# Kernel tuning notes

Measured on AMD Instinct MI355X. Metric: run time of the kernel, lower is better.

## Reference

```python
import jax, jax.numpy as jnp
import numpy as np
from jax import lax

N_NODES = 100000
N_EDGES = 3200000
NODE_DIM = 128
K = 8            # number of kmeans heads
MAX_OVERLAP = 2  # top-k cluster memberships per node
THRESH = 1e-8


def setup_inputs() -> dict:
    key = jax.random.key(0)
    k1, k2, k3, k4, k5 = jax.random.split(key, 5)
    x = jax.random.normal(k1, (N_NODES, NODE_DIM), dtype=jnp.float32)
    edge_index = jax.random.randint(k2, (2, N_EDGES), 0, N_NODES, dtype=jnp.int64)
    # binary initial cluster-membership masks [N, K] (float, like KMeansCarry.mask)
    mask = (jax.random.uniform(k3, (N_NODES, K)) > 0.5).astype(jnp.float32)
    Ww = jax.random.normal(k4, (K, NODE_DIM, NODE_DIM), dtype=jnp.float32) * (1.0 / np.sqrt(NODE_DIM))
    Wm = jax.random.normal(k5, (K, NODE_DIM, 1), dtype=jnp.float32) * (1.0 / np.sqrt(NODE_DIM))
    return {"x": x, "edge_index": edge_index, "mask": mask, "Ww": Ww, "Wm": Wm}


def reference(x, edge_index, mask, Ww, Wm):
    """KMeans over graph: k heads -> boolean node scores -> norm-weighted top-k assignment."""
    N = x.shape[0]
    src, dst = edge_index[0], edge_index[1]

    def head(m_col, Ww_i, Wm_i):
        # masked node features (KMeansCarry.masked_x)
        xm = x * m_col[:, None]                                   # [N, D]
        node_mask = m_col > 0                                     # [N]
        # masked subgraph (KMeansCarry.masked_edge_index): keep edges with both endpoints in mask
        ev = (node_mask[src] & node_mask[dst]).astype(x.dtype)    # [E]
        # weighting module: per-node transform
        w = jax.nn.relu(xm @ Ww_i)                                # [N, D]
        # message passing over masked subgraph (irregular gather/scatter)
        agg = jax.ops.segment_sum(w[src] * ev[:, None], dst, num_segments=N)  # [N, D]
        # mask module score -> act -> threshold at 0 (KMeansHead.forward)
        score = ((xm + agg) @ Wm_i)[:, 0]                         # [N]
        return jnp.tanh(score) > 0                                # bool [N]

    # vmap over the K heads
    head_masks = jax.vmap(head, in_axes=(1, 0, 0), out_axes=1)(mask, Ww, Wm)  # [N, K] bool

    # KMeans.forward combine step
    above_thresh = head_masks  # bool > THRESH (1e-8 < 1) == the bool itself
    norms = jnp.linalg.norm(x, axis=1, keepdims=True)             # [N, 1]
    masked_weights = jnp.where(above_thresh, norms, -jnp.inf)     # [N, K]
    top_vals, top_idx = lax.top_k(masked_weights, MAX_OVERLAP)    # [N, MAX_OVERLAP]
    valid = jnp.isfinite(top_vals)
    # scatter ones at (row, top_idx) where valid  (duplicate-safe via one-hot + min)
    oh = jax.nn.one_hot(top_idx, K, dtype=x.dtype) * valid[..., None].astype(x.dtype)
    final_mask = jnp.minimum(oh.sum(axis=1), 1.0)                 # [N, K]
    return final_mask
```

## Files before the change

kernel.cpp:

```cpp
#include <hip/hip_runtime.h>

#define N_NODES 100000
#define N_EDGES 3200000
#define D 128
#define K 8

#define TAU 4e-3f
#define WL_CAP 262144

#define CHUNK 128
#define GWAVES 8

#define BKT 256
#define NB  ((N_NODES + BKT - 1) / BKT)
#define EPB 16384
#define NEB ((N_EDGES + EPB - 1) / EPB)

typedef float  f32x4  __attribute__((ext_vector_type(4)));
typedef __bf16 bf16x8 __attribute__((ext_vector_type(8)));

static __device__ __forceinline__ unsigned short bfbits(float f)
{
    const __bf16 b = (__bf16)f;
    return __builtin_bit_cast(unsigned short, b);
}
static __device__ __forceinline__ float bfback(unsigned short u)
{
    return (float)__builtin_bit_cast(__bf16, u);
}

__global__ __launch_bounds__(256)
void compact_kernel(const float* __restrict__ mask,
                    int* __restrict__ lists,
                    int* __restrict__ cnts,
                    unsigned char* __restrict__ mb)
{
    __shared__ int wcnt[4][K];
    __shared__ int wbase[4][K];

    const int n = blockIdx.x * 256 + threadIdx.x;
    const int lane = threadIdx.x & 63;
    const int wave = threadIdx.x >> 6;
    const bool valid = (n < N_NODES);

    unsigned long long ball[K];
    int bits8 = 0;
    #pragma unroll
    for (int k = 0; k < K; ++k) {
        const bool m = valid && (mask[(size_t)n * K + k] > 0.0f);
        bits8 |= m ? (1 << k) : 0;
        ball[k] = __ballot(m);
        if (lane == 0) wcnt[wave][k] = __popcll(ball[k]);
    }
    __syncthreads();

    if (threadIdx.x < K) {
        const int k = threadIdx.x;
        const int t0 = wcnt[0][k], t1 = wcnt[1][k], t2 = wcnt[2][k], t3 = wcnt[3][k];
        const int base = (t0 + t1 + t2 + t3)
                       ? atomicAdd(&cnts[k], t0 + t1 + t2 + t3) : 0;
        wbase[0][k] = base;
        wbase[1][k] = base + t0;
        wbase[2][k] = base + t0 + t1;
        wbase[3][k] = base + t0 + t1 + t2;
    }
    __syncthreads();

    #pragma unroll
    for (int k = 0; k < K; ++k) {
        if ((ball[k] >> lane) & 1ull) {
            const int pos = __popcll(ball[k] & ((1ull << lane) - 1ull));
            lists[(size_t)k * N_NODES + wbase[wave][k] + pos] = n;
        }
    }
    if (valid) mb[n] = (unsigned char)bits8;
}

__global__ __launch_bounds__(256)
void wsplit_kernel(const float* __restrict__ Ww,
                   unsigned short* __restrict__ wtH,
                   unsigned short* __restrict__ wtL)
{
    const int t = blockIdx.x * 256 + threadIdx.x;
    if (t >= K * D * D) return;
    const int k   = t >> 14;
    const int kk  = (t >> 7) & 127;
    const int col = t & 127;
    const float v = Ww[t];
    const __bf16 h = (__bf16)v;
    const __bf16 l = (__bf16)(v - (float)h);
    const int o = (k << 14) | (col << 7) | kk;
    wtH[o] = __builtin_bit_cast(unsigned short, h);
    wtL[o] = __builtin_bit_cast(unsigned short, l);
}

__global__ __launch_bounds__(512, 4)
void head_gemm_kernel(const float* __restrict__ x,
                      const unsigned short* __restrict__ wtH,
                      const unsigned short* __restrict__ wtL,
                      const float* __restrict__ Wm,
                      const int* __restrict__ lists,
                      const int* __restrict__ cnts,
                      float* __restrict__ t32,
                      float* __restrict__ base32)
{
    __shared__ __align__(16) unsigned short Ah[CHUNK * D];
    __shared__ __align__(16) unsigned short Al[CHUNK * D];
    __shared__ float redT[GWAVES][64];
    __shared__ float redB[CHUNK][4];
    __shared__ int   ids[CHUNK];

    const int bid = blockIdx.x;
    const int k = (bid >> 3) & 7;
    const int c = ((bid >> 6) << 3) | (bid & 7);

    const int cnt = cnts[k];
    const int nbase = c * CHUNK;
    if (nbase >= cnt) return;

    const int tid = threadIdx.x;
    const int lane = tid & 63;
    const int wave = __builtin_amdgcn_readfirstlane((int)(tid >> 6));
    const int* list = lists + (size_t)k * N_NODES;

    if (tid < CHUNK) {
        int idx = nbase + tid;
        if (idx >= cnt) idx = cnt - 1;
        ids[tid] = list[idx];
    }
    __syncthreads();

    {
        const int r = tid >> 2;
        const int q = tid & 3;
        const int id = ids[r];
        const float4* xr  = (const float4*)(x + (size_t)id * D);
        const float4* wm4 = (const float4*)(Wm + k * D);
        float bp = 0.0f;
        #pragma unroll
        for (int i = 0; i < 8; ++i) {
            const int f4 = q + 4 * i;
            const float4 v  = xr[f4];
            const float4 wv = wm4[f4];
            bp += v.x * wv.x + v.y * wv.y + v.z * wv.z + v.w * wv.w;
            ushort4 h, l;
            h.x = bfbits(v.x); l.x = bfbits(v.x - bfback(h.x));
            h.y = bfbits(v.y); l.y = bfbits(v.y - bfback(h.y));
            h.z = bfbits(v.z); l.z = bfbits(v.z - bfback(h.z));
            h.w = bfbits(v.w); l.w = bfbits(v.w - bfback(h.w));
            const int boff = ((r * 256 + f4 * 8) ^ ((r & 7) << 4)) >> 1;
            *(ushort4*)&Ah[boff] = h;
            *(ushort4*)&Al[boff] = l;
        }
        redB[r][q] = bp;
    }
    __syncthreads();

    const int wm_ = wave >> 2;
    const int wn  = wave & 3;
    const int l15 = lane & 15;
    const int lg  = lane >> 4;
    const int n0  = wn * 32;

    f32x4 acc[4][2];
    #pragma unroll
    for (int mf = 0; mf < 4; ++mf) {
        acc[mf][0] = (f32x4){0.f, 0.f, 0.f, 0.f};
        acc[mf][1] = (f32x4){0.f, 0.f, 0.f, 0.f};
    }

    const unsigned short* bH0 = wtH + (((k * D + n0 + l15) << 7) + 8 * lg);
    const unsigned short* bH1 = bH0 + (16 << 7);
    const unsigned short* bL0 = wtL + (((k * D + n0 + l15) << 7) + 8 * lg);
    const unsigned short* bL1 = bL0 + (16 << 7);

    #pragma unroll
    for (int s = 0; s < 4; ++s) {
        const int ko = s * 32;
        const bf16x8 Bh0 = *reinterpret_cast<const bf16x8*>(bH0 + ko);
        const bf16x8 Bh1 = *reinterpret_cast<const bf16x8*>(bH1 + ko);
        const bf16x8 Bl0 = *reinterpret_cast<const bf16x8*>(bL0 + ko);
        const bf16x8 Bl1 = *reinterpret_cast<const bf16x8*>(bL1 + ko);
        #pragma unroll
        for (int mf = 0; mf < 4; ++mf) {
            const int m = wm_ * 64 + mf * 16 + l15;
            const int byt = (m * 256 + (ko + 8 * lg) * 2) ^ ((m & 7) << 4);
            const bf16x8 Amh = *reinterpret_cast<const bf16x8*>(&Ah[byt >> 1]);
            const bf16x8 Aml = *reinterpret_cast<const bf16x8*>(&Al[byt >> 1]);
            acc[mf][0] = __builtin_amdgcn_mfma_f32_16x16x32_bf16(Amh, Bh0, acc[mf][0], 0, 0, 0);
            acc[mf][1] = __builtin_amdgcn_mfma_f32_16x16x32_bf16(Amh, Bh1, acc[mf][1], 0, 0, 0);
            acc[mf][0] = __builtin_amdgcn_mfma_f32_16x16x32_bf16(Amh, Bl0, acc[mf][0], 0, 0, 0);
            acc[mf][1] = __builtin_amdgcn_mfma_f32_16x16x32_bf16(Amh, Bl1, acc[mf][1], 0, 0, 0);
            acc[mf][0] = __builtin_amdgcn_mfma_f32_16x16x32_bf16(Aml, Bh0, acc[mf][0], 0, 0, 0);
            acc[mf][1] = __builtin_amdgcn_mfma_f32_16x16x32_bf16(Aml, Bh1, acc[mf][1], 0, 0, 0);
        }
    }

    const float wmv0 = Wm[k * D + n0 + l15];
    const float wmv1 = Wm[k * D + n0 + 16 + l15];
    float keep = 0.0f;
    #pragma unroll
    for (int mf = 0; mf < 4; ++mf) {
        #pragma unroll
        for (int r = 0; r < 4; ++r) {
            float p = fmaxf(acc[mf][0][r], 0.0f) * wmv0
                    + fmaxf(acc[mf][1][r], 0.0f) * wmv1;
            p += __shfl_xor(p, 1);
            p += __shfl_xor(p, 2);
            p += __shfl_xor(p, 4);
            p += __shfl_xor(p, 8);
            if (l15 == mf * 4 + r) keep = p;
        }
    }
    redT[wave][((l15 >> 2) << 4) + (lg << 2) + (l15 & 3)] = keep;
    __syncthreads();

    if (tid < CHUNK) {
        const int r = tid;
        const int idx = nbase + r;
        if (idx < cnt) {
            const int wg = r >> 6;
            const int rl = r & 63;
            const float ts = redT[wg * 4 + 0][rl] + redT[wg * 4 + 1][rl]
                           + redT[wg * 4 + 2][rl] + redT[wg * 4 + 3][rl];
            const float bs = redB[r][0] + redB[r][1] + redB[r][2] + redB[r][3];
            const int id = ids[r];
            t32[(size_t)id * K + k]    = ts;
            base32[(size_t)id * K + k] = bs;
        }
    }
}

__global__ __launch_bounds__(256)
void ehist_kernel(const int* __restrict__ ei, int* __restrict__ bhist)
{
    __shared__ int lh[NB];
    const int tid = threadIdx.x;
    for (int i = tid; i < NB; i += 256) lh[i] = 0;
    __syncthreads();
    const int e0 = blockIdx.x * EPB;
    #pragma unroll 4
    for (int i = 0; i < EPB / 256; ++i) {
        const int e = e0 + i * 256 + tid;
        if (e < N_EDGES) {
            const int d = ei[(long long)N_EDGES + e];
            atomicAdd(&lh[d >> 8], 1);
        }
    }
    __syncthreads();
    for (int i = tid; i < NB; i += 256) {
        const int c = lh[i];
        if (c) atomicAdd(&bhist[i], c);
    }
}

__global__ __launch_bounds__(512)
void escan_kernel(const int* __restrict__ bhist,
                  int* __restrict__ bases,
                  int* __restrict__ cursors)
{
    __shared__ int sc[512];
    const int tid = threadIdx.x;
    const int v = (tid < NB) ? bhist[tid] : 0;
    sc[tid] = v;
    __syncthreads();
    for (int off = 1; off < 512; off <<= 1) {
        int t = 0;
        if (tid >= off) t = sc[tid - off];
        __syncthreads();
        sc[tid] += t;
        __syncthreads();
    }
    if (tid < NB) {
        const int ex = sc[tid] - v;
        bases[tid]   = ex;
        cursors[tid] = ex;
        if (tid == NB - 1) bases[NB] = sc[tid];
    }
}

__global__ __launch_bounds__(256)
void ebucket_kernel(const int* __restrict__ ei,
                    int* __restrict__ cursors,
                    int* __restrict__ bkt)
{
    __shared__ int lh[NB];
    __shared__ int wb[NB];
    const int tid = threadIdx.x;
    for (int i = tid; i < NB; i += 256) lh[i] = 0;
    __syncthreads();
    const int e0 = blockIdx.x * EPB;
    #pragma unroll 4
    for (int i = 0; i < EPB / 256; ++i) {
        const int e = e0 + i * 256 + tid;
        if (e < N_EDGES) atomicAdd(&lh[ei[(long long)N_EDGES + e] >> 8], 1);
    }
    __syncthreads();
    for (int i = tid; i < NB; i += 256) {
        const int c = lh[i];
        wb[i] = c ? atomicAdd(&cursors[i], c) : 0;
        lh[i] = 0;
    }
    __syncthreads();
    #pragma unroll 4
    for (int i = 0; i < EPB / 256; ++i) {
        const int e = e0 + i * 256 + tid;
        if (e < N_EDGES) {
            const int d = ei[(long long)N_EDGES + e];
            const int s = ei[e];
            const int b = d >> 8;
            const int r = atomicAdd(&lh[b], 1);
            const int idx = wb[b] + r;
            if (idx < N_EDGES)
                bkt[idx] = (s << 8) | (d & 255);
        }
    }
}

__global__ __launch_bounds__(512)
void eaccum_kernel(const int* __restrict__ bkt,
                   const int* __restrict__ bases,
                   const unsigned char* __restrict__ mb,
                   const float* __restrict__ t32,
                   const float* __restrict__ base32,
                   float* __restrict__ agg32,
                   float* __restrict__ out,
                   unsigned char* __restrict__ flag8,
                   double* __restrict__ s64,
                   int2* __restrict__ wl,
                   int* __restrict__ wlcnt)
{
    __shared__ float acc[BKT * K];
    __shared__ unsigned char mbl[BKT];
    __shared__ unsigned char fll[BKT];
    __shared__ int anyfl;
    const int b = blockIdx.x;
    const int n0 = b << 8;
    const int tid = threadIdx.x;
    for (int i = tid; i < BKT * K; i += 512) acc[i] = 0.0f;
    if (tid < BKT) {
        const int n = n0 + tid;
        mbl[tid] = (n < N_NODES) ? mb[n] : 0;
    }
    if (tid == 0) anyfl = 0;
    __syncthreads();

    const int eB = bases[b];
    int eE = bases[b + 1];
    if (eE > N_EDGES) eE = N_EDGES;
    for (int e = eB + tid; e < eE; e += 512) {
        const int rec = bkt[e];
        const int s  = rec >> 8;
        const int dl = rec & 255;
        const unsigned md = mbl[dl] & mb[s];
        if (md) {
            const float4* tr = (const float4*)(t32 + (size_t)s * K);
            const float4 t0 = tr[0], t1 = tr[1];
            #pragma unroll
            for (int k = 0; k < K; ++k) {
                const float tv = (k < 4)
                    ? ((k < 2) ? (k == 0 ? t0.x : t0.y) : (k == 2 ? t0.z : t0.w))
                    : ((k < 6) ? (k == 4 ? t1.x : t1.y) : (k == 6 ? t1.z : t1.w));
                if (((md >> k) & 1) && tv != 0.0f)
                    atomicAdd(&acc[(dl << 3) + k], tv);
            }
        }
    }
    __syncthreads();

    if (tid < BKT) {
        const int n = n0 + tid;
        if (n < N_NODES) {
            const unsigned m8 = mbl[tid];
            const float4* b4 = (const float4*)(base32 + (size_t)n * K);
            const float4 b40 = b4[0], b41 = b4[1];
            float bs[K];
            bs[0] = b40.x; bs[1] = b40.y; bs[2] = b40.z; bs[3] = b40.w;
            bs[4] = b41.x; bs[5] = b41.y; bs[6] = b41.z; bs[7] = b41.w;
            float o[K];
            int cnt = 0, fl = 0;
            #pragma unroll
            for (int k = 0; k < K; ++k) {
                const float sc = bs[k] + acc[(tid << 3) + k];
                const bool masked = (m8 >> k) & 1;
                const bool hm = masked && (sc > 0.0f);
                if (masked && fabsf(sc) < TAU) fl |= (1 << k);
                o[k] = (hm && cnt < 2) ? 1.0f : 0.0f;
                cnt += hm ? 1 : 0;
            }
            float4* op = (float4*)(out + (size_t)n * K);
            op[0] = make_float4(o[0], o[1], o[2], o[3]);
            op[1] = make_float4(o[4], o[5], o[6], o[7]);
            float4* ap = (float4*)(agg32 + (size_t)n * K);
            ap[0] = make_float4(acc[(tid << 3) + 0], acc[(tid << 3) + 1],
                                acc[(tid << 3) + 2], acc[(tid << 3) + 3]);
            ap[1] = make_float4(acc[(tid << 3) + 4], acc[(tid << 3) + 5],
                                acc[(tid << 3) + 6], acc[(tid << 3) + 7]);
            flag8[n] = (unsigned char)fl;
            fll[tid] = (unsigned char)fl;
            if (fl) {
                anyfl = 1;
                #pragma unroll
                for (int k = 0; k < K; ++k)
                    if ((fl >> k) & 1) s64[(size_t)n * K + k] = 0.0;
            }
        } else {
            fll[tid] = 0;
        }
    }
    __syncthreads();

    if (anyfl) {
        for (int e = eB + tid; e < eE; e += 512) {
            const int rec = bkt[e];
            const int dl = rec & 255;
            unsigned f = fll[dl];
            if (!f) continue;
            const int s = rec >> 8;
            f &= mb[s];
            while (f) {
                const int k = __ffs(f) - 1;
                f &= f - 1;
                const int idx = atomicAdd(wlcnt, 1);
                if (idx < WL_CAP) wl[idx] = make_int2(s | (k << 20), n0 + dl);
            }
        }
    }
}

__global__ __launch_bounds__(256)
void scatter_fallback_kernel(const int* __restrict__ ei,
                             const unsigned char* __restrict__ mb,
                             const float* __restrict__ t32,
                             float* __restrict__ agg32)
{
    const long long tid = (long long)blockIdx.x * 256 + threadIdx.x;
    if (tid >= (long long)N_EDGES * K) return;
    const int k = (int)(tid & (K - 1));
    const long long e = tid >> 3;
    const int d = ei[(long long)N_EDGES + e];
    const int s = ei[e];
    const unsigned md = mb[d] & mb[s];
    if (!((md >> k) & 1)) return;
    const float v = t32[(size_t)s * K + k];
    if (v != 0.0f) atomicAdd(&agg32[(size_t)d * K + k], v);
}

__global__ __launch_bounds__(256)
void combine_flag_kernel(const unsigned char* __restrict__ mb,
                         const float* __restrict__ base32,
                         const float* __restrict__ agg32,
                         float* __restrict__ out,
                         unsigned char* __restrict__ flag8,
                         double* __restrict__ s64)
{
    const int n = blockIdx.x * 256 + threadIdx.x;
    if (n >= N_NODES) return;
    const unsigned m8 = mb[n];
    float o[K];
    int cnt = 0, fl = 0;
    #pragma unroll
    for (int k = 0; k < K; ++k) {
        const float s = base32[(size_t)n * K + k] + agg32[(size_t)n * K + k];
        const bool masked = (m8 >> k) & 1;
        const bool hm = masked && (s > 0.0f);
        if (masked && fabsf(s) < TAU) fl |= (1 << k);
        o[k] = (hm && cnt < 2) ? 1.0f : 0.0f;
        cnt += hm ? 1 : 0;
    }
    float4* op = (float4*)(out + (size_t)n * K);
    op[0] = make_float4(o[0], o[1], o[2], o[3]);
    op[1] = make_float4(o[4], o[5], o[6], o[7]);
    flag8[n] = (unsigned char)fl;
    if (fl) {
        #pragma unroll
        for (int k = 0; k < K; ++k)
            if ((fl >> k) & 1) s64[(size_t)n * K + k] = 0.0;
    }
}

__global__ __launch_bounds__(256)
void edge_flag_kernel(const int* __restrict__ ei,
                      const unsigned char* __restrict__ mb,
                      const unsigned char* __restrict__ flag8,
                      int2* __restrict__ wl,
                      int* __restrict__ wlcnt)
{
    const int e = blockIdx.x * 256 + threadIdx.x;
    if (e >= N_EDGES) return;
    const int d = ei[(long long)N_EDGES + e];
    unsigned f = flag8[d];
    if (!f) return;
    const int s = ei[e];
    f &= mb[s];
    while (f) {
        const int k = __ffs(f) - 1;
        f &= f - 1;
        const int idx = atomicAdd(wlcnt, 1);
        if (idx < WL_CAP) wl[idx] = make_int2(s | (k << 20), d);
    }
}

__global__ __launch_bounds__(256)
void repair_t_kernel(const float* __restrict__ x,
                     const float* __restrict__ Ww,
                     const float* __restrict__ Wm,
                     const int2* __restrict__ wl,
                     const int* __restrict__ wlcnt,
                     double* __restrict__ score64)
{
    const int lane = threadIdx.x & 63;
    const int waveId = blockIdx.x * 4 + (threadIdx.x >> 6);
    const int nWaves = gridDim.x * 4;
    int cnt = *wlcnt;
    if (cnt > WL_CAP) cnt = WL_CAP;
    for (int w = waveId; w < cnt; w += nWaves) {
        const int2 ent = wl[w];
        const int s = __builtin_amdgcn_readfirstlane(ent.x & 0xFFFFF);
        const int k = __builtin_amdgcn_readfirstlane(ent.x >> 20);
        const int d = ent.y;
        const float* xr = x + (size_t)s * D;
        const float* Wk = Ww + (size_t)k * D * D;
        double c0 = 0.0, c1 = 0.0;
        for (int j = 0; j < D; ++j) {
            const double xd = (double)xr[j];
            c0 = fma(xd, (double)Wk[j * D + lane], c0);
            c1 = fma(xd, (double)Wk[j * D + lane + 64], c1);
        }
        double ts = fmax(c0, 0.0) * (double)Wm[k * D + lane]
                  + fmax(c1, 0.0) * (double)Wm[k * D + lane + 64];
        #pragma unroll
        for (int off = 32; off > 0; off >>= 1) ts += __shfl_xor(ts, off);
        if (lane == 0) atomicAdd(&score64[(size_t)d * K + k], ts);
    }
}

__global__ __launch_bounds__(256)
void repair_combine_kernel(const float* __restrict__ x,
                           const unsigned char* __restrict__ mb,
                           const float* __restrict__ Wm,
                           const float* __restrict__ base32,
                           const float* __restrict__ agg32,
                           const double* __restrict__ score64,
                           const unsigned char* __restrict__ flag8,
                           float* __restrict__ out)
{
    const int n = blockIdx.x * 256 + threadIdx.x;
    if (n >= N_NODES) return;
    const unsigned f = flag8[n];
    if (!f) return;
    const unsigned m8 = mb[n];
    float o[K];
    int cnt = 0;
    #pragma unroll
    for (int k = 0; k < K; ++k) {
        bool hm;
        if ((f >> k) & 1) {
            double b = 0.0;
            for (int j = 0; j < D; ++j)
                b = fma((double)x[(size_t)n * D + j], (double)Wm[k * D + j], b);
            hm = (b + score64[(size_t)n * K + k]) > 0.0;
        } else {
            hm = ((m8 >> k) & 1) &&
                 ((base32[(size_t)n * K + k] + agg32[(size_t)n * K + k]) > 0.0f);
        }
        o[k] = (hm && cnt < 2) ? 1.0f : 0.0f;
        cnt += hm ? 1 : 0;
    }
    float4* op = (float4*)(out + (size_t)n * K);
    op[0] = make_float4(o[0], o[1], o[2], o[3]);
    op[1] = make_float4(o[4], o[5], o[6], o[7]);
}

extern "C" void kernel_launch(void* const* d_in, const int* in_sizes, int n_in,
                              void* d_out, int out_size, void* d_ws, size_t ws_size,
                              hipStream_t stream)
{
    const float* x    = (const float*)d_in[0];
    const int*   ei   = (const int*)d_in[1];
    const float* mask = (const float*)d_in[2];
    const float* Ww   = (const float*)d_in[3];
    const float* Wm   = (const float*)d_in[4];
    float* out = (float*)d_out;

    char* w = (char*)d_ws;
    float*          t32    = (float*)w;
    float*          agg32  = (float*)(w + 3200000);
    double*         s64    = (double*)(w + 6400000);
    int*            lists  = (int*)(w + 6400000);
    unsigned short* wtH    = (unsigned short*)(w + 9600000);
    unsigned short* wtL    = (unsigned short*)(w + 9600000 + 262144);
    unsigned char*  flag8  = (unsigned char*)(w + 12800000);
    int*            cnts   = (int*)(w + 12900000);
    int*            wlcnt  = (int*)(w + 12900032);
    int*            bhist  = (int*)(w + 12900064);
    int*            bases  = (int*)(w + 12901632);
    int*            cursors= (int*)(w + 12903200);
    int2*           wl     = (int2*)(w + 12904768);
    float*          b32    = (float*)(w + 15001920);
    unsigned char*  mb     = (unsigned char*)(w + 18201920);
    int*            bkt    = (int*)(w + 18301920);
    const size_t WS_BUCKETED = 31101920;
    const bool bucketed = (ws_size >= WS_BUCKETED);

    hipMemsetAsync(w + 12900000, 0, 4096, stream);

    wsplit_kernel<<<(K * D * D + 255) / 256, 256, 0, stream>>>(Ww, wtH, wtL);

    compact_kernel<<<(N_NODES + 255) / 256, 256, 0, stream>>>(mask, lists, cnts, mb);

    const int nchunks = (N_NODES + CHUNK - 1) / CHUNK;
    const int nc8 = (nchunks + 7) & ~7;
    head_gemm_kernel<<<nc8 * K, 512, 0, stream>>>(x, wtH, wtL, Wm, lists, cnts, t32, b32);

    if (bucketed) {
        ehist_kernel<<<NEB, 256, 0, stream>>>(ei, bhist);
        escan_kernel<<<1, 512, 0, stream>>>(bhist, bases, cursors);
        ebucket_kernel<<<NEB, 256, 0, stream>>>(ei, cursors, bkt);
        eaccum_kernel<<<NB, 512, 0, stream>>>(bkt, bases, mb, t32, b32,
                                              agg32, out, flag8, s64, wl, wlcnt);
    } else {
        hipMemsetAsync(agg32, 0, 3200000, stream);
        const long long nek = (long long)N_EDGES * K;
        scatter_fallback_kernel<<<(int)((nek + 255) / 256), 256, 0, stream>>>(
            ei, mb, t32, agg32);
        combine_flag_kernel<<<(N_NODES + 255) / 256, 256, 0, stream>>>(
            mb, b32, agg32, out, flag8, s64);
        edge_flag_kernel<<<(N_EDGES + 255) / 256, 256, 0, stream>>>(
            ei, mb, flag8, wl, wlcnt);
    }

    repair_t_kernel<<<512, 256, 0, stream>>>(x, Ww, Wm, wl, wlcnt, s64);

    repair_combine_kernel<<<(N_NODES + 255) / 256, 256, 0, stream>>>(
        x, mb, Wm, b32, agg32, s64, flag8, out);
}
```

Measured before the change: 389.3 us.

## Replace per-head compacted GEMM with dense all-head GEMM per node chunk

Drops the per-head compaction of masked nodes and the gathered head GEMM. Each block now loads a contiguous chunk of x once, splits it to bf16 hi/lo in shared memory, and loops over all 8 heads. It also computes the x·Wm base term with an extra MFMA against a pre-split Wm. The aim is to stop re-reading x once per head through scattered gathers, remove the atomic list building, and allow coalesced float4 stores of t32 and base32. In exchange it computes every head for every node, roughly doubling MFMA work, and launches far fewer blocks, each running a serialized head loop with barriers.

```diff
diff --git a/kernel.cpp b/kernel.cpp
--- a/kernel.cpp
+++ b/kernel.cpp
@@ -30,50 +30,23 @@
 }
 
 __global__ __launch_bounds__(256)
-void compact_kernel(const float* __restrict__ mask,
-                    int* __restrict__ lists,
-                    int* __restrict__ cnts,
-                    unsigned char* __restrict__ mb)
-{
-    __shared__ int wcnt[4][K];
-    __shared__ int wbase[4][K];
-
+void mask_kernel(const float* __restrict__ mask,
+                 unsigned char* __restrict__ mb)
+{
     const int n = blockIdx.x * 256 + threadIdx.x;
-    const int lane = threadIdx.x & 63;
-    const int wave = threadIdx.x >> 6;
-    const bool valid = (n < N_NODES);
-
-    unsigned long long ball[K];
+    if (n >= N_NODES) return;
+    const float4* m4 = (const float4*)(mask + (size_t)n * K);
+    const float4 a = m4[0], b = m4[1];
     int bits8 = 0;
-    #pragma unroll
-    for (int k = 0; k < K; ++k) {
-        const bool m = valid && (mask[(size_t)n * K + k] > 0.0f);
-        bits8 |= m ? (1 << k) : 0;
-        ball[k] = __ballot(m);
-        if (lane == 0) wcnt[wave][k] = __popcll(ball[k]);
-    }
-    __syncthreads();
-
-    if (threadIdx.x < K) {
-        const int k = threadIdx.x;
-        const int t0 = wcnt[0][k], t1 = wcnt[1][k], t2 = wcnt[2][k], t3 = wcnt[3][k];
-        const int base = (t0 + t1 + t2 + t3)
-                       ? atomicAdd(&cnts[k], t0 + t1 + t2 + t3) : 0;
-        wbase[0][k] = base;
-        wbase[1][k] = base + t0;
-        wbase[2][k] = base + t0 + t1;
-        wbase[3][k] = base + t0 + t1 + t2;
-    }
-    __syncthreads();
-
-    #pragma unroll
-    for (int k = 0; k < K; ++k) {
-        if ((ball[k] >> lane) & 1ull) {
-            const int pos = __popcll(ball[k] & ((1ull << lane) - 1ull));
-            lists[(size_t)k * N_NODES + wbase[wave][k] + pos] = n;
-        }
-    }
-    if (valid) mb[n] = (unsigned char)bits8;
+    bits8 |= (a.x > 0.0f) ? 1   : 0;
+    bits8 |= (a.y > 0.0f) ? 2   : 0;
+    bits8 |= (a.z > 0.0f) ? 4   : 0;
+    bits8 |= (a.w > 0.0f) ? 8   : 0;
+    bits8 |= (b.x > 0.0f) ? 16  : 0;
+    bits8 |= (b.y > 0.0f) ? 32  : 0;
+    bits8 |= (b.z > 0.0f) ? 64  : 0;
+    bits8 |= (b.w > 0.0f) ? 128 : 0;
+    mb[n] = (unsigned char)bits8;
 }
 
 __global__ __launch_bounds__(256)
@@ -94,55 +67,53 @@
     wtL[o] = __builtin_bit_cast(unsigned short, l);
 }
 
+__global__ __launch_bounds__(256)
+void wmsplit_kernel(const float* __restrict__ Wm,
+                    unsigned short* __restrict__ wmtH,
+                    unsigned short* __restrict__ wmtL)
+{
+    const int t = blockIdx.x * 256 + threadIdx.x;
+    if (t >= 16 * D) return;
+    const int col = t >> 7;
+    const int j   = t & 127;
+    const float v = (col < K) ? Wm[col * D + j] : 0.0f;
+    const __bf16 h = (__bf16)v;
+    const __bf16 l = (__bf16)(v - (float)h);
+    wmtH[t] = __builtin_bit_cast(unsigned short, h);
+    wmtL[t] = __builtin_bit_cast(unsigned short, l);
+}
+
 __global__ __launch_bounds__(512, 4)
 void head_gemm_kernel(const float* __restrict__ x,
                       const unsigned short* __restrict__ wtH,
                       const unsigned short* __restrict__ wtL,
+                      const unsigned short* __restrict__ wmtH,
+                      const unsigned short* __restrict__ wmtL,
                       const float* __restrict__ Wm,
-                      const int* __restrict__ lists,
-                      const int* __restrict__ cnts,
                       float* __restrict__ t32,
                       float* __restrict__ base32)
 {
     __shared__ __align__(16) unsigned short Ah[CHUNK * D];
     __shared__ __align__(16) unsigned short Al[CHUNK * D];
     __shared__ float redT[GWAVES][64];
-    __shared__ float redB[CHUNK][4];
-    __shared__ int   ids[CHUNK];
-
-    const int bid = blockIdx.x;
-    const int k = (bid >> 3) & 7;
-    const int c = ((bid >> 6) << 3) | (bid & 7);
-
-    const int cnt = cnts[k];
-    const int nbase = c * CHUNK;
-    if (nbase >= cnt) return;
-
+    __shared__ float tout[CHUNK][K];
+    __shared__ float bout[CHUNK][K];
+
+    const int n0 = blockIdx.x * CHUNK;
     const int tid = threadIdx.x;
     const int lane = tid & 63;
     const int wave = __builtin_amdgcn_readfirstlane((int)(tid >> 6));
-    const int* list = lists + (size_t)k * N_NODES;
-
-    if (tid < CHUNK) {
-        int idx = nbase + tid;
-        if (idx >= cnt) idx = cnt - 1;
-        ids[tid] = list[idx];
-    }
-    __syncthreads();
 
     {
         const int r = tid >> 2;
         const int q = tid & 3;
-        const int id = ids[r];
-        const float4* xr  = (const float4*)(x + (size_t)id * D);
-        const float4* wm4 = (const float4*)(Wm + k * D);
-        float bp = 0.0f;
+        int n = n0 + r;
+        if (n >= N_NODES) n = N_NODES - 1;
+        const float4* xr = (const float4*)(x + (size_t)n * D);
         #pragma unroll
         for (int i = 0; i < 8; ++i) {
             const int f4 = q + 4 * i;
-            const float4 v  = xr[f4];
-            const float4 wv = wm4[f4];
-            bp += v.x * wv.x + v.y * wv.y + v.z * wv.z + v.w * wv.w;
+            const float4 v = xr[f4];
             ushort4 h, l;
             h.x = bfbits(v.x); l.x = bfbits(v.x - bfback(h.x));
             h.y = bfbits(v.y); l.y = bfbits(v.y - bfback(h.y));
@@ -152,81 +123,110 @@
             *(ushort4*)&Ah[boff] = h;
             *(ushort4*)&Al[boff] = l;
         }
-        redB[r][q] = bp;
-    }
-    __syncthreads();
-
-    const int wm_ = wave >> 2;
-    const int wn  = wave & 3;
+    }
+    __syncthreads();
+
     const int l15 = lane & 15;
     const int lg  = lane >> 4;
-    const int n0  = wn * 32;
-
-    f32x4 acc[4][2];
-    #pragma unroll
-    for (int mf = 0; mf < 4; ++mf) {
-        acc[mf][0] = (f32x4){0.f, 0.f, 0.f, 0.f};
-        acc[mf][1] = (f32x4){0.f, 0.f, 0.f, 0.f};
-    }
-
-    const unsigned short* bH0 = wtH + (((k * D + n0 + l15) << 7) + 8 * lg);
-    const unsigned short* bH1 = bH0 + (16 << 7);
-    const unsigned short* bL0 = wtL + (((k * D + n0 + l15) << 7) + 8 * lg);
-    const unsigned short* bL1 = bL0 + (16 << 7);
-
-    #pragma unroll
-    for (int s = 0; s < 4; ++s) {
-        const int ko = s * 32;
-        const bf16x8 Bh0 = *reinterpret_cast<const bf16x8*>(bH0 + ko);
-        const bf16x8 Bh1 = *reinterpret_cast<const bf16x8*>(bH1 + ko);
-        const bf16x8 Bl0 = *reinterpret_cast<const bf16x8*>(bL0 + ko);
-        const bf16x8 Bl1 = *reinterpret_cast<const bf16x8*>(bL1 + ko);
+
+    {
+        f32x4 bacc = (f32x4){0.f, 0.f, 0.f, 0.f};
+        const unsigned short* bmh = wmtH + (l15 << 7) + 8 * lg;
+        const unsigned short* bml = wmtL + (l15 << 7) + 8 * lg;
+        const int m = wave * 16 + l15;
         #pragma unroll
-        for (int mf = 0; mf < 4; ++mf) {
-            const int m = wm_ * 64 + mf * 16 + l15;
+        for (int s = 0; s < 4; ++s) {
+            const int ko = s * 32;
+            const bf16x8 Bh = *reinterpret_cast<const bf16x8*>(bmh + ko);
+            const bf16x8 Bl = *reinterpret_cast<const bf16x8*>(bml + ko);
             const int byt = (m * 256 + (ko + 8 * lg) * 2) ^ ((m & 7) << 4);
             const bf16x8 Amh = *reinterpret_cast<const bf16x8*>(&Ah[byt >> 1]);
             const bf16x8 Aml = *reinterpret_cast<const bf16x8*>(&Al[byt >> 1]);
-            acc[mf][0] = __builtin_amdgcn_mfma_f32_16x16x32_bf16(Amh, Bh0, acc[mf][0], 0, 0, 0);
-            acc[mf][1] = __builtin_amdgcn_mfma_f32_16x16x32_bf16(Amh, Bh1, acc[mf][1], 0, 0, 0);
-            acc[mf][0] = __builtin_amdgcn_mfma_f32_16x16x32_bf16(Amh, Bl0, acc[mf][0], 0, 0, 0);
-            acc[mf][1] = __builtin_amdgcn_mfma_f32_16x16x32_bf16(Amh, Bl1, acc[mf][1], 0, 0, 0);
-            acc[mf][0] = __builtin_amdgcn_mfma_f32_16x16x32_bf16(Aml, Bh0, acc[mf][0], 0, 0, 0);
-            acc[mf][1] = __builtin_amdgcn_mfma_f32_16x16x32_bf16(Aml, Bh1, acc[mf][1], 0, 0, 0);
-        }
-    }
-
-    const float wmv0 = Wm[k * D + n0 + l15];
-    const float wmv1 = Wm[k * D + n0 + 16 + l15];
-    float keep = 0.0f;
-    #pragma unroll
-    for (int mf = 0; mf < 4; ++mf) {
+            bacc = __builtin_amdgcn_mfma_f32_16x16x32_bf16(Amh, Bh, bacc, 0, 0, 0);
+            bacc = __builtin_amdgcn_mfma_f32_16x16x32_bf16(Amh, Bl, bacc, 0, 0, 0);
+            bacc = __builtin_amdgcn_mfma_f32_16x16x32_bf16(Aml, Bh, bacc, 0, 0, 0);
+        }
+        if (l15 < K) {
+            #pragma unroll
+            for (int r = 0; r < 4; ++r)
+                bout[wave * 16 + lg * 4 + r][l15] = bacc[r];
+        }
+    }
+
+    const int wm_ = wave >> 2;
+    const int wn  = wave & 3;
+    const int nn0 = wn * 32;
+
+    for (int k = 0; k < K; ++k) {
+        f32x4 acc[4][2];
         #pragma unroll
-        for (int r = 0; r < 4; ++r) {
-            float p = fmaxf(acc[mf][0][r], 0.0f) * wmv0
-                    + fmaxf(acc[mf][1][r], 0.0f) * wmv1;
-            p += __shfl_xor(p, 1);
-            p += __shfl_xor(p, 2);
-            p += __shfl_xor(p, 4);
-            p += __shfl_xor(p, 8);
-            if (l15 == mf * 4 + r) keep = p;
-        }
-    }
-    redT[wave][((l15 >> 2) << 4) + (lg << 2) + (l15 & 3)] = keep;
-    __syncthreads();
+        for (int mf = 0; mf < 4; ++mf) {
+            acc[mf][0] = (f32x4){0.f, 0.f, 0.f, 0.f};
+            acc[mf][1] = (f32x4){0.f, 0.f, 0.f, 0.f};
+        }
+        const unsigned short* bH0 = wtH + (((k * D + nn0 + l15) << 7) + 8 * lg);
+        const unsigned short* bH1 = bH0 + (16 << 7);
+        const unsigned short* bL0 = wtL + (((k * D + nn0 + l15) << 7) + 8 * lg);
+        const unsigned short* bL1 = bL0 + (16 << 7);
+
+        #pragma unroll
+        for (int s = 0; s < 4; ++s) {
+            const int ko = s * 32;
+            const bf16x8 Bh0 = *reinterpret_cast<const bf16x8*>(bH0 + ko);
+            const bf16x8 Bh1 = *reinterpret_cast<const bf16x8*>(bH1 + ko);
+            const bf16x8 Bl0 = *reinterpret_cast<const bf16x8*>(bL0 + ko);
+            const bf16x8 Bl1 = *reinterpret_cast<const bf16x8*>(bL1 + ko);
+            #pragma unroll
+            for (int mf = 0; mf < 4; ++mf) {
+                const int m = wm_ * 64 + mf * 16 + l15;
+                const int byt = (m * 256 + (ko + 8 * lg) * 2) ^ ((m & 7) << 4);
+                const bf16x8 Amh = *reinterpret_cast<const bf16x8*>(&Ah[byt >> 1]);
+                const bf16x8 Aml = *reinterpret_cast<const bf16x8*>(&Al[byt >> 1]);
+                acc[mf][0] = __builtin_amdgcn_mfma_f32_16x16x32_bf16(Amh, Bh0, acc[mf][0], 0, 0, 0);
+                acc[mf][1] = __builtin_amdgcn_mfma_f32_16x16x32_bf16(Amh, Bh1, acc[mf][1], 0, 0, 0);
+                acc[mf][0] = __builtin_amdgcn_mfma_f32_16x16x32_bf16(Amh, Bl0, acc[mf][0], 0, 0, 0);
+                acc[mf][1] = __builtin_amdgcn_mfma_f32_16x16x32_bf16(Amh, Bl1, acc[mf][1], 0, 0, 0);
+                acc[mf][0] = __builtin_amdgcn_mfma_f32_16x16x32_bf16(Aml, Bh0, acc[mf][0], 0, 0, 0);
+                acc[mf][1] = __builtin_amdgcn_mfma_f32_16x16x32_bf16(Aml, Bh1, acc[mf][1], 0, 0, 0);
+            }
+        }
+
+        const float wmv0 = Wm[k * D + nn0 + l15];
+        const float wmv1 = Wm[k * D + nn0 + 16 + l15];
+        float keep = 0.0f;
+        #pragma unroll
+        for (int mf = 0; mf < 4; ++mf) {
+            #pragma unroll
+            for (int r = 0; r < 4; ++r) {
+                float p = fmaxf(acc[mf][0][r], 0.0f) * wmv0
+                        + fmaxf(acc[mf][1][r], 0.0f) * wmv1;
+                p += __shfl_xor(p, 1);
+                p += __shfl_xor(p, 2);
+                p += __shfl_xor(p, 4);
+                p += __shfl_xor(p, 8);
+                if (l15 == mf * 4 + r) keep = p;
+            }
+        }
+        redT[wave][((l15 >> 2) << 4) + (lg << 2) + (l15 & 3)] = keep;
+        __syncthreads();
+        if (tid < CHUNK) {
+            const int wg = tid >> 6;
+            const int rl = tid & 63;
+            tout[tid][k] = redT[wg * 4 + 0][rl] + redT[wg * 4 + 1][rl]
+                         + redT[wg * 4 + 2][rl] + redT[wg * 4 + 3][rl];
+        }
+        __syncthreads();
+    }
 
     if (tid < CHUNK) {
-        const int r = tid;
-        const int idx = nbase + r;
-        if (idx < cnt) {
-            const int wg = r >> 6;
-            const int rl = r & 63;
-            const float ts = redT[wg * 4 + 0][rl] + redT[wg * 4 + 1][rl]
-                           + redT[wg * 4 + 2][rl] + redT[wg * 4 + 3][rl];
-            const float bs = redB[r][0] + redB[r][1] + redB[r][2] + redB[r][3];
-            const int id = ids[r];
-            t32[(size_t)id * K + k]    = ts;
-            base32[(size_t)id * K + k] = bs;
+        const int n = n0 + tid;
+        if (n < N_NODES) {
+            float4* tp = (float4*)(t32 + (size_t)n * K);
+            tp[0] = make_float4(tout[tid][0], tout[tid][1], tout[tid][2], tout[tid][3]);
+            tp[1] = make_float4(tout[tid][4], tout[tid][5], tout[tid][6], tout[tid][7]);
+            float4* bp = (float4*)(base32 + (size_t)n * K);
+            bp[0] = make_float4(bout[tid][0], bout[tid][1], bout[tid][2], bout[tid][3]);
+            bp[1] = make_float4(bout[tid][4], bout[tid][5], bout[tid][6], bout[tid][7]);
         }
     }
 }
@@ -587,11 +587,11 @@
     float*          t32    = (float*)w;
     float*          agg32  = (float*)(w + 3200000);
     double*         s64    = (double*)(w + 6400000);
-    int*            lists  = (int*)(w + 6400000);
     unsigned short* wtH    = (unsigned short*)(w + 9600000);
     unsigned short* wtL    = (unsigned short*)(w + 9600000 + 262144);
+    unsigned short* wmtH   = (unsigned short*)(w + 10124288);
+    unsigned short* wmtL   = (unsigned short*)(w + 10128384);
     unsigned char*  flag8  = (unsigned char*)(w + 12800000);
-    int*            cnts   = (int*)(w + 12900000);
     int*            wlcnt  = (int*)(w + 12900032);
     int*            bhist  = (int*)(w + 12900064);
     int*            bases  = (int*)(w + 12901632);
@@ -606,12 +606,13 @@
     hipMemsetAsync(w + 12900000, 0, 4096, stream);
 
     wsplit_kernel<<<(K * D * D + 255) / 256, 256, 0, stream>>>(Ww, wtH, wtL);
-
-    compact_kernel<<<(N_NODES + 255) / 256, 256, 0, stream>>>(mask, lists, cnts, mb);
+    wmsplit_kernel<<<(16 * D + 255) / 256, 256, 0, stream>>>(Wm, wmtH, wmtL);
+
+    mask_kernel<<<(N_NODES + 255) / 256, 256, 0, stream>>>(mask, mb);
 
     const int nchunks = (N_NODES + CHUNK - 1) / CHUNK;
-    const int nc8 = (nchunks + 7) & ~7;
-    head_gemm_kernel<<<nc8 * K, 512, 0, stream>>>(x, wtH, wtL, Wm, lists, cnts, t32, b32);
+    head_gemm_kernel<<<nchunks, 512, 0, stream>>>(x, wtH, wtL, wmtH, wmtL,
+                                                  Wm, t32, b32);
 
     if (bucketed) {
         ehist_kernel<<<NEB, 256, 0, stream>>>(ei, bhist);
```

Result: slower. 438.1 us (+12.5%).
